# Kernel tuning notes

Hardware: AMD Instinct MI355X
Metric: run time of the kernel (lower is better)

## Reference

```python
import jax, jax.numpy as jnp
import numpy as np


def _gcn(x, src, dst, W, b, n):
    # symmetric normalization: deg computed on edges WITH self-loops (weights 1)
    deg = jax.ops.segment_sum(jnp.ones_like(src, dtype=x.dtype), dst, num_segments=n)
    dinv = jnp.where(deg > 0, jax.lax.rsqrt(deg), 0.0)
    norm = dinv[src] * dinv[dst]              # [E+n]
    xw = x @ W                                # [n, out] transform first (cheaper)
    msg = xw[src] * norm[:, None]             # gather + edge scale
    return jax.ops.segment_sum(msg, dst, num_segments=n) + b


def setup_inputs() -> dict:
    key = jax.random.key(0)
    ks = jax.random.split(key, 8)
    N, E = 100_000, 1_280_000
    x = jax.random.normal(ks[0], (N, 18), dtype=jnp.float32)
    edge_index = jax.random.randint(ks[1], (2, E), 0, N, dtype=jnp.int32)
    W1 = jax.random.normal(ks[2], (18, 32), dtype=jnp.float32) * 0.2
    b1 = jnp.zeros((32,), dtype=jnp.float32)
    W2 = jax.random.normal(ks[3], (32, 64), dtype=jnp.float32) * 0.15
    b2 = jnp.zeros((64,), dtype=jnp.float32)
    Wfc = jax.random.normal(ks[4], (64, 2), dtype=jnp.float32) * 0.1
    bfc = jnp.zeros((2,), dtype=jnp.float32)
    return {"x": x, "edge_index": edge_index, "W1": W1, "b1": b1,
            "W2": W2, "b2": b2, "Wfc": Wfc, "bfc": bfc}


def reference(x, edge_index, W1, b1, W2, b2, Wfc, bfc):
    n = x.shape[0]
    loop = jnp.arange(n, dtype=edge_index.dtype)
    src = jnp.concatenate([edge_index[0], loop])   # add self-loops (PyG default)
    dst = jnp.concatenate([edge_index[1], loop])
    h = jax.nn.relu(_gcn(x, src, dst, W1, b1, n))
    h = jax.nn.relu(_gcn(h, src, dst, W2, b2, n))
    logits = h @ Wfc + bfc
    return jax.nn.log_softmax(logits, axis=1)
```

## Files before the change

kernel.cpp:

```cpp
#include <hip/hip_runtime.h>
#include <hip/hip_fp16.h>
#include <math.h>


#define TPB 256
#define BSH 8
#define BNODES 256
#define MAXBUCK 512
#define CH 8192
#define NPW 8
#define CAPSH 12
#define CAP (1 << CAPSH)

__global__ void k_initcur(int* __restrict__ bcursor, int nbuck) {
    int i = blockIdx.x * blockDim.x + threadIdx.x;
    if (i < nbuck) bcursor[i] = i << CAPSH;
}

__global__ void k_part(const int* __restrict__ src, const int* __restrict__ dst,
                       int* __restrict__ bcursor, int* __restrict__ eb,
                       int E, int nbuck) {
    __shared__ int lh[MAXBUCK];
    __shared__ int lbase[MAXBUCK];
    int t = threadIdx.x;
    int chunk0 = blockIdx.x * CH;
    int end = min(chunk0 + CH, E);
    const int4* dst4 = (const int4*)dst;
    const int4* src4 = (const int4*)src;
    for (int i = t; i < nbuck; i += TPB) lh[i] = 0;
    __syncthreads();
    for (int e4 = chunk0 / 4 + t; e4 * 4 < end; e4 += TPB) {
        int base = e4 * 4;
        int4 d = dst4[e4];
        if (base + 0 < end) atomicAdd(&lh[d.x >> BSH], 1);
        if (base + 1 < end) atomicAdd(&lh[d.y >> BSH], 1);
        if (base + 2 < end) atomicAdd(&lh[d.z >> BSH], 1);
        if (base + 3 < end) atomicAdd(&lh[d.w >> BSH], 1);
    }
    __syncthreads();
    for (int i = t; i < nbuck; i += TPB) {
        int c = lh[i];
        lbase[i] = c ? atomicAdd(&bcursor[i], c) : 0;
        lh[i] = 0;
    }
    __syncthreads();
    for (int e4 = chunk0 / 4 + t; e4 * 4 < end; e4 += TPB) {
        int base = e4 * 4;
        int4 d = dst4[e4];
        int4 s = src4[e4];
        #define PUT(c, sv) if (base + c < end) { \
            int b = (d.sv) >> BSH; \
            int r = atomicAdd(&lh[b], 1); \
            int pos = lbase[b] + r; \
            if (pos < ((b + 1) << CAPSH)) \
                eb[pos] = ((s.sv) << BSH) | ((d.sv) & (BNODES - 1)); }
        PUT(0, x) PUT(1, y) PUT(2, z) PUT(3, w)
        #undef PUT
    }
}

__global__ void k_bucket(const int* __restrict__ eb, const int* __restrict__ bcursor,
                         const float* __restrict__ x,
                         int* __restrict__ csr, int* __restrict__ row_start,
                         int* __restrict__ cnt, float* __restrict__ dinv,
                         __half* __restrict__ u1h, int n) {
    __shared__ int lcnt[BNODES];
    __shared__ int lscan[BNODES];
    __shared__ float ldinv[BNODES];
    int b = blockIdx.x;
    int t = threadIdx.x;
    int node0 = b << BSH;
    int beg = b << CAPSH;
    int end = bcursor[b];
    lcnt[t] = 0;
    __syncthreads();
    for (int i = beg + t; i < end; i += TPB)
        atomicAdd(&lcnt[eb[i] & (BNODES - 1)], 1);
    __syncthreads();
    int v = lcnt[t];
    lscan[t] = v;
    __syncthreads();
    for (int off = 1; off < TPB; off <<= 1) {
        int xx = (t >= off) ? lscan[t - off] : 0;
        __syncthreads();
        lscan[t] += xx;
        __syncthreads();
    }
    int excl = lscan[t] - v;
    int node = node0 + t;
    float dv = rsqrtf(1.0f + (float)v);
    ldinv[t] = dv;
    if (node < n) {
        row_start[node] = beg + excl;
        cnt[node] = v;
        dinv[node] = dv;
    }
    __syncthreads();
    lcnt[t] = excl;
    __syncthreads();
    for (int i = beg + t; i < end; i += TPB) {
        int e = eb[i];
        int p = atomicAdd(&lcnt[e & (BNODES - 1)], 1);
        csr[beg + p] = e >> BSH;
    }
    int nn = min(BNODES, n - node0);
    int tot = nn * 32;
    const float* xb = x + (size_t)node0 * 18;
    __half* ub = u1h + (size_t)node0 * 32;
    for (int i = t; i < tot; i += TPB) {
        int nl = i >> 5, f = i & 31;
        float val = (f < 18) ? xb[nl * 18 + f] * ldinv[nl] : 0.f;
        ub[i] = __float2half_rn(val);
    }
}

template <int OS, int NW>
__global__ void k_agg(const __half2* __restrict__ uh2, const int* __restrict__ row_start,
                      const int* __restrict__ cnt, const int* __restrict__ csr,
                      float* __restrict__ agg, int n) {
    int t = blockIdx.x * blockDim.x + threadIdx.x;
    int node = t >> 4, f2 = t & 15;
    if (node >= n) return;
    int beg = row_start[node], num = cnt[node];
    float2 acc = __half22float2(uh2[(size_t)node * 16 + f2]);
    int i = 0;
    for (; i + 4 <= num; i += 4) {
        int s0 = csr[beg + i], s1 = csr[beg + i + 1];
        int s2 = csr[beg + i + 2], s3 = csr[beg + i + 3];
        float2 v0 = __half22float2(uh2[(size_t)s0 * 16 + f2]);
        float2 v1 = __half22float2(uh2[(size_t)s1 * 16 + f2]);
        float2 v2 = __half22float2(uh2[(size_t)s2 * 16 + f2]);
        float2 v3 = __half22float2(uh2[(size_t)s3 * 16 + f2]);
        acc.x += (v0.x + v1.x) + (v2.x + v3.x);
        acc.y += (v0.y + v1.y) + (v2.y + v3.y);
    }
    for (; i < num; ++i) {
        int s = csr[beg + i];
        float2 v = __half22float2(uh2[(size_t)s * 16 + f2]);
        acc.x += v.x;
        acc.y += v.y;
    }
    if (f2 < NW) *(float2*)(agg + (size_t)node * OS + 2 * f2) = acc;
}

__global__ void k_l1(const float* __restrict__ agg1, const float* __restrict__ W1,
                     const float* __restrict__ dinv, const float* __restrict__ b1,
                     __half* __restrict__ u2h, int n) {
    int lane = threadIdx.x & 63;
    int f = lane & 31;
    int wid = __builtin_amdgcn_readfirstlane((int)(threadIdx.x >> 6));
    int wave = blockIdx.x * (TPB / 64) + wid;
    float w1r[18];
#pragma unroll
    for (int k = 0; k < 18; ++k) w1r[k] = W1[k * 32 + f];
    float b1v = b1[f];
    int node0 = wave * NPW;
    for (int r = 0; r < NPW; ++r) {
        int node = node0 + r;
        if (node >= n) return;
        const float* rp = agg1 + (size_t)node * 18;
        float a = 0.f;
#pragma unroll
        for (int k = 0; k < 18; ++k) a = fmaf(rp[k], w1r[k], a);
        float di = dinv[node];
        if (lane < 32)
            u2h[(size_t)node * 32 + f] =
                __float2half_rn(fmaxf(fmaf(di, a, b1v), 0.f) * di);
    }
}

__global__ void k_l2_out(const float* __restrict__ agg2, const float* __restrict__ W2,
                         const float* __restrict__ dinv, const float* __restrict__ b2,
                         const float* __restrict__ Wfc, const float* __restrict__ bfc,
                         float* __restrict__ out, int n) {
    int lane = threadIdx.x & 63;
    int wid = __builtin_amdgcn_readfirstlane((int)(threadIdx.x >> 6));
    int wave = blockIdx.x * (TPB / 64) + wid;
    float w2r[32];
#pragma unroll
    for (int k = 0; k < 32; ++k) w2r[k] = W2[k * 64 + lane];
    float b2v = b2[lane];
    float wf0 = Wfc[lane * 2 + 0], wf1 = Wfc[lane * 2 + 1];
    float bf0 = bfc[0], bf1 = bfc[1];
    int node0 = wave * NPW;
    for (int r = 0; r < NPW; ++r) {
        int node = node0 + r;
        if (node >= n) return;
        const float* rp = agg2 + (size_t)node * 32;
        float a0 = 0.f, a1 = 0.f, a2 = 0.f, a3 = 0.f;
#pragma unroll
        for (int k = 0; k < 32; k += 4) {
            a0 = fmaf(rp[k],     w2r[k],     a0);
            a1 = fmaf(rp[k + 1], w2r[k + 1], a1);
            a2 = fmaf(rp[k + 2], w2r[k + 2], a2);
            a3 = fmaf(rp[k + 3], w2r[k + 3], a3);
        }
        float a = (a0 + a1) + (a2 + a3);
        float v = fmaxf(fmaf(dinv[node], a, b2v), 0.f);
        float l0 = v * wf0;
        float l1 = v * wf1;
#pragma unroll
        for (int off = 32; off >= 1; off >>= 1) {
            l0 += __shfl_xor(l0, off, 64);
            l1 += __shfl_xor(l1, off, 64);
        }
        if (lane == 0) {
            l0 += bf0;
            l1 += bf1;
            float m2 = fmaxf(l0, l1);
            float lse = m2 + logf(expf(l0 - m2) + expf(l1 - m2));
            out[node * 2 + 0] = l0 - lse;
            out[node * 2 + 1] = l1 - lse;
        }
    }
}

extern "C" void kernel_launch(void* const* d_in, const int* in_sizes, int n_in,
                              void* d_out, int out_size, void* d_ws, size_t ws_size,
                              hipStream_t stream) {
    const float* x   = (const float*)d_in[0];
    const int*   ei  = (const int*)d_in[1];
    const float* W1  = (const float*)d_in[2];
    const float* b1  = (const float*)d_in[3];
    const float* W2  = (const float*)d_in[4];
    const float* b2  = (const float*)d_in[5];
    const float* Wfc = (const float*)d_in[6];
    const float* bfc = (const float*)d_in[7];
    float* out = (float*)d_out;

    const int n = in_sizes[0] / 18;
    const int E = in_sizes[1] / 2;
    const int* src = ei;
    const int* dst = ei + E;
    const int nbuck = (n + BNODES - 1) >> BSH;

    char* w = (char*)d_ws;
    int*    bcursor   = (int*)w;     w += (size_t)nbuck * 4;
    int*    row_start = (int*)w;     w += (size_t)n * 4;
    int*    cnt       = (int*)w;     w += (size_t)n * 4;
    float*  dinv      = (float*)w;   w += (size_t)n * 4;
    int*    eb        = (int*)w;     w += (size_t)nbuck * CAP * 4;
    int*    csr       = (int*)w;     w += (size_t)nbuck * CAP * 4;
    float*  agg1      = (float*)w;   w += (size_t)n * 18 * 4;
    float*  agg2      = (float*)w;   w += (size_t)n * 32 * 4;
    w = (char*)(((size_t)w + 63) & ~(size_t)63);
    __half* u1h       = (__half*)w;  w += (size_t)n * 32 * 2;
    w = (char*)(((size_t)w + 63) & ~(size_t)63);
    __half* u2h       = (__half*)w;  w += (size_t)n * 32 * 2;

    auto blocks = [](long long work) { return (int)((work + TPB - 1) / TPB); };

    k_initcur<<<blocks(nbuck), TPB, 0, stream>>>(bcursor, nbuck);
    k_part<<<(E + CH - 1) / CH, TPB, 0, stream>>>(src, dst, bcursor, eb, E, nbuck);
    k_bucket<<<nbuck, TPB, 0, stream>>>(eb, bcursor, x, csr, row_start, cnt, dinv, u1h, n);

    const int blocksA = blocks((long long)n * 16);
    const int wavesT = (n + NPW - 1) / NPW;
    const int blocksT = (wavesT + (TPB / 64) - 1) / (TPB / 64);

    k_agg<18, 9><<<blocksA, TPB, 0, stream>>>((const __half2*)u1h, row_start, cnt, csr, agg1, n);
    k_l1<<<blocksT, TPB, 0, stream>>>(agg1, W1, dinv, b1, u2h, n);

    k_agg<32, 16><<<blocksA, TPB, 0, stream>>>((const __half2*)u2h, row_start, cnt, csr, agg2, n);
    k_l2_out<<<blocksT, TPB, 0, stream>>>(agg2, W2, dinv, b2, Wfc, bfc, out, n);
}
```

Measured before the change: 196.5 us.

## Fuse neighbor aggregation with dense transforms and replace cursor init with memset

Each layer's gather-aggregation kernel is merged with its dense transform kernel. The aggregated features for 16 nodes are staged in shared memory, and the same block then applies W1 (or W2 plus the FC and log-softmax) in a grid-stride loop. This removes the agg1/agg2 global round trips and two launches. The per-bucket cursor now counts from zero, set by a memset in place of an init kernel, and bucket offsets are computed from the bucket index. The cost is block-level syncs per group, a persistent grid capped at 2048 blocks, and register pressure from the held weights.

```diff
diff --git a/kernel.cpp b/kernel.cpp
--- a/kernel.cpp
+++ b/kernel.cpp
@@ -8,14 +8,8 @@
 #define BNODES 256
 #define MAXBUCK 512
 #define CH 8192
-#define NPW 8
 #define CAPSH 12
 #define CAP (1 << CAPSH)
-
-__global__ void k_initcur(int* __restrict__ bcursor, int nbuck) {
-    int i = blockIdx.x * blockDim.x + threadIdx.x;
-    if (i < nbuck) bcursor[i] = i << CAPSH;
-}
 
 __global__ void k_part(const int* __restrict__ src, const int* __restrict__ dst,
                        int* __restrict__ bcursor, int* __restrict__ eb,
@@ -50,10 +44,9 @@
         int4 s = src4[e4];
         #define PUT(c, sv) if (base + c < end) { \
             int b = (d.sv) >> BSH; \
-            int r = atomicAdd(&lh[b], 1); \
-            int pos = lbase[b] + r; \
-            if (pos < ((b + 1) << CAPSH)) \
-                eb[pos] = ((s.sv) << BSH) | ((d.sv) & (BNODES - 1)); }
+            int r = lbase[b] + atomicAdd(&lh[b], 1); \
+            if (r < CAP) \
+                eb[((size_t)b << CAPSH) + r] = ((s.sv) << BSH) | ((d.sv) & (BNODES - 1)); }
         PUT(0, x) PUT(1, y) PUT(2, z) PUT(3, w)
         #undef PUT
     }
@@ -71,7 +64,7 @@
     int t = threadIdx.x;
     int node0 = b << BSH;
     int beg = b << CAPSH;
-    int end = bcursor[b];
+    int end = beg + min(bcursor[b], CAP);
     lcnt[t] = 0;
     __syncthreads();
     for (int i = beg + t; i < end; i += TPB)
@@ -114,104 +107,141 @@
     }
 }
 
-template <int OS, int NW>
-__global__ void k_agg(const __half2* __restrict__ uh2, const int* __restrict__ row_start,
-                      const int* __restrict__ cnt, const int* __restrict__ csr,
-                      float* __restrict__ agg, int n) {
-    int t = blockIdx.x * blockDim.x + threadIdx.x;
-    int node = t >> 4, f2 = t & 15;
-    if (node >= n) return;
-    int beg = row_start[node], num = cnt[node];
-    float2 acc = __half22float2(uh2[(size_t)node * 16 + f2]);
-    int i = 0;
-    for (; i + 4 <= num; i += 4) {
-        int s0 = csr[beg + i], s1 = csr[beg + i + 1];
-        int s2 = csr[beg + i + 2], s3 = csr[beg + i + 3];
-        float2 v0 = __half22float2(uh2[(size_t)s0 * 16 + f2]);
-        float2 v1 = __half22float2(uh2[(size_t)s1 * 16 + f2]);
-        float2 v2 = __half22float2(uh2[(size_t)s2 * 16 + f2]);
-        float2 v3 = __half22float2(uh2[(size_t)s3 * 16 + f2]);
-        acc.x += (v0.x + v1.x) + (v2.x + v3.x);
-        acc.y += (v0.y + v1.y) + (v2.y + v3.y);
-    }
-    for (; i < num; ++i) {
-        int s = csr[beg + i];
-        float2 v = __half22float2(uh2[(size_t)s * 16 + f2]);
-        acc.x += v.x;
-        acc.y += v.y;
-    }
-    if (f2 < NW) *(float2*)(agg + (size_t)node * OS + 2 * f2) = acc;
-}
-
-__global__ void k_l1(const float* __restrict__ agg1, const float* __restrict__ W1,
-                     const float* __restrict__ dinv, const float* __restrict__ b1,
-                     __half* __restrict__ u2h, int n) {
-    int lane = threadIdx.x & 63;
+__global__ void k_fused1(const __half2* __restrict__ u1h2, const int* __restrict__ row_start,
+                         const int* __restrict__ cnt, const int* __restrict__ csr,
+                         const float* __restrict__ dinv, const float* __restrict__ W1,
+                         const float* __restrict__ b1, __half* __restrict__ u2h,
+                         int n, int ngroups) {
+    __shared__ float lagg[16][19];
+    int t = threadIdx.x;
+    int lane = t & 63, wv = t >> 6;
+    int f2 = t & 15, nl = t >> 4;
     int f = lane & 31;
-    int wid = __builtin_amdgcn_readfirstlane((int)(threadIdx.x >> 6));
-    int wave = blockIdx.x * (TPB / 64) + wid;
     float w1r[18];
 #pragma unroll
     for (int k = 0; k < 18; ++k) w1r[k] = W1[k * 32 + f];
     float b1v = b1[f];
-    int node0 = wave * NPW;
-    for (int r = 0; r < NPW; ++r) {
-        int node = node0 + r;
-        if (node >= n) return;
-        const float* rp = agg1 + (size_t)node * 18;
-        float a = 0.f;
-#pragma unroll
-        for (int k = 0; k < 18; ++k) a = fmaf(rp[k], w1r[k], a);
-        float di = dinv[node];
-        if (lane < 32)
-            u2h[(size_t)node * 32 + f] =
-                __float2half_rn(fmaxf(fmaf(di, a, b1v), 0.f) * di);
-    }
-}
-
-__global__ void k_l2_out(const float* __restrict__ agg2, const float* __restrict__ W2,
-                         const float* __restrict__ dinv, const float* __restrict__ b2,
-                         const float* __restrict__ Wfc, const float* __restrict__ bfc,
-                         float* __restrict__ out, int n) {
-    int lane = threadIdx.x & 63;
-    int wid = __builtin_amdgcn_readfirstlane((int)(threadIdx.x >> 6));
-    int wave = blockIdx.x * (TPB / 64) + wid;
+    for (int g = blockIdx.x; g < ngroups; g += gridDim.x) {
+        int node = g * 16 + nl;
+        float2 acc = make_float2(0.f, 0.f);
+        if (node < n) {
+            acc = __half22float2(u1h2[(size_t)node * 16 + f2]);
+            int beg = row_start[node], num = cnt[node];
+            int i = 0;
+            for (; i + 4 <= num; i += 4) {
+                int s0 = csr[beg + i], s1 = csr[beg + i + 1];
+                int s2 = csr[beg + i + 2], s3 = csr[beg + i + 3];
+                float2 v0 = __half22float2(u1h2[(size_t)s0 * 16 + f2]);
+                float2 v1 = __half22float2(u1h2[(size_t)s1 * 16 + f2]);
+                float2 v2 = __half22float2(u1h2[(size_t)s2 * 16 + f2]);
+                float2 v3 = __half22float2(u1h2[(size_t)s3 * 16 + f2]);
+                acc.x += (v0.x + v1.x) + (v2.x + v3.x);
+                acc.y += (v0.y + v1.y) + (v2.y + v3.y);
+            }
+            for (; i < num; ++i) {
+                int s = csr[beg + i];
+                float2 v = __half22float2(u1h2[(size_t)s * 16 + f2]);
+                acc.x += v.x;
+                acc.y += v.y;
+            }
+        }
+        if (f2 < 9) {
+            lagg[nl][2 * f2] = acc.x;
+            lagg[nl][2 * f2 + 1] = acc.y;
+        }
+        __syncthreads();
+#pragma unroll
+        for (int rr = 0; rr < 4; ++rr) {
+            int nl2 = rr * 4 + wv;
+            int node2 = g * 16 + nl2;
+            if (node2 < n) {
+                float a = 0.f;
+#pragma unroll
+                for (int k = 0; k < 18; ++k) a = fmaf(lagg[nl2][k], w1r[k], a);
+                float di = dinv[node2];
+                if (lane < 32)
+                    u2h[(size_t)node2 * 32 + f] =
+                        __float2half_rn(fmaxf(fmaf(di, a, b1v), 0.f) * di);
+            }
+        }
+        __syncthreads();
+    }
+}
+
+__global__ void k_fused2(const __half2* __restrict__ u2h2, const int* __restrict__ row_start,
+                         const int* __restrict__ cnt, const int* __restrict__ csr,
+                         const float* __restrict__ dinv, const float* __restrict__ W2,
+                         const float* __restrict__ b2, const float* __restrict__ Wfc,
+                         const float* __restrict__ bfc, float* __restrict__ out,
+                         int n, int ngroups) {
+    __shared__ float lagg[16][33];
+    int t = threadIdx.x;
+    int lane = t & 63, wv = t >> 6;
+    int f2 = t & 15, nl = t >> 4;
     float w2r[32];
 #pragma unroll
     for (int k = 0; k < 32; ++k) w2r[k] = W2[k * 64 + lane];
     float b2v = b2[lane];
     float wf0 = Wfc[lane * 2 + 0], wf1 = Wfc[lane * 2 + 1];
     float bf0 = bfc[0], bf1 = bfc[1];
-    int node0 = wave * NPW;
-    for (int r = 0; r < NPW; ++r) {
-        int node = node0 + r;
-        if (node >= n) return;
-        const float* rp = agg2 + (size_t)node * 32;
-        float a0 = 0.f, a1 = 0.f, a2 = 0.f, a3 = 0.f;
-#pragma unroll
-        for (int k = 0; k < 32; k += 4) {
-            a0 = fmaf(rp[k],     w2r[k],     a0);
-            a1 = fmaf(rp[k + 1], w2r[k + 1], a1);
-            a2 = fmaf(rp[k + 2], w2r[k + 2], a2);
-            a3 = fmaf(rp[k + 3], w2r[k + 3], a3);
-        }
-        float a = (a0 + a1) + (a2 + a3);
-        float v = fmaxf(fmaf(dinv[node], a, b2v), 0.f);
-        float l0 = v * wf0;
-        float l1 = v * wf1;
-#pragma unroll
-        for (int off = 32; off >= 1; off >>= 1) {
-            l0 += __shfl_xor(l0, off, 64);
-            l1 += __shfl_xor(l1, off, 64);
-        }
-        if (lane == 0) {
-            l0 += bf0;
-            l1 += bf1;
-            float m2 = fmaxf(l0, l1);
-            float lse = m2 + logf(expf(l0 - m2) + expf(l1 - m2));
-            out[node * 2 + 0] = l0 - lse;
-            out[node * 2 + 1] = l1 - lse;
-        }
+    for (int g = blockIdx.x; g < ngroups; g += gridDim.x) {
+        int node = g * 16 + nl;
+        float2 acc = make_float2(0.f, 0.f);
+        if (node < n) {
+            acc = __half22float2(u2h2[(size_t)node * 16 + f2]);
+            int beg = row_start[node], num = cnt[node];
+            int i = 0;
+            for (; i + 4 <= num; i += 4) {
+                int s0 = csr[beg + i], s1 = csr[beg + i + 1];
+                int s2 = csr[beg + i + 2], s3 = csr[beg + i + 3];
+                float2 v0 = __half22float2(u2h2[(size_t)s0 * 16 + f2]);
+                float2 v1 = __half22float2(u2h2[(size_t)s1 * 16 + f2]);
+                float2 v2 = __half22float2(u2h2[(size_t)s2 * 16 + f2]);
+                float2 v3 = __half22float2(u2h2[(size_t)s3 * 16 + f2]);
+                acc.x += (v0.x + v1.x) + (v2.x + v3.x);
+                acc.y += (v0.y + v1.y) + (v2.y + v3.y);
+            }
+            for (; i < num; ++i) {
+                int s = csr[beg + i];
+                float2 v = __half22float2(u2h2[(size_t)s * 16 + f2]);
+                acc.x += v.x;
+                acc.y += v.y;
+            }
+        }
+        lagg[nl][2 * f2] = acc.x;
+        lagg[nl][2 * f2 + 1] = acc.y;
+        __syncthreads();
+#pragma unroll
+        for (int rr = 0; rr < 4; ++rr) {
+            int nl2 = rr * 4 + wv;
+            int node2 = g * 16 + nl2;
+            float a0 = 0.f, a1 = 0.f, a2 = 0.f, a3 = 0.f;
+#pragma unroll
+            for (int k = 0; k < 32; k += 4) {
+                a0 = fmaf(lagg[nl2][k],     w2r[k],     a0);
+                a1 = fmaf(lagg[nl2][k + 1], w2r[k + 1], a1);
+                a2 = fmaf(lagg[nl2][k + 2], w2r[k + 2], a2);
+                a3 = fmaf(lagg[nl2][k + 3], w2r[k + 3], a3);
+            }
+            float a = (a0 + a1) + (a2 + a3);
+            float v = (node2 < n) ? fmaxf(fmaf(dinv[node2], a, b2v), 0.f) : 0.f;
+            float l0 = v * wf0;
+            float l1 = v * wf1;
+#pragma unroll
+            for (int off = 32; off >= 1; off >>= 1) {
+                l0 += __shfl_xor(l0, off, 64);
+                l1 += __shfl_xor(l1, off, 64);
+            }
+            if (lane == 0 && node2 < n) {
+                l0 += bf0;
+                l1 += bf1;
+                float m2 = fmaxf(l0, l1);
+                float lse = m2 + logf(expf(l0 - m2) + expf(l1 - m2));
+                out[node2 * 2 + 0] = l0 - lse;
+                out[node2 * 2 + 1] = l1 - lse;
+            }
+        }
+        __syncthreads();
     }
 }
 
@@ -241,26 +271,20 @@
     float*  dinv      = (float*)w;   w += (size_t)n * 4;
     int*    eb        = (int*)w;     w += (size_t)nbuck * CAP * 4;
     int*    csr       = (int*)w;     w += (size_t)nbuck * CAP * 4;
-    float*  agg1      = (float*)w;   w += (size_t)n * 18 * 4;
-    float*  agg2      = (float*)w;   w += (size_t)n * 32 * 4;
     w = (char*)(((size_t)w + 63) & ~(size_t)63);
     __half* u1h       = (__half*)w;  w += (size_t)n * 32 * 2;
     w = (char*)(((size_t)w + 63) & ~(size_t)63);
     __half* u2h       = (__half*)w;  w += (size_t)n * 32 * 2;
 
-    auto blocks = [](long long work) { return (int)((work + TPB - 1) / TPB); };
-
-    k_initcur<<<blocks(nbuck), TPB, 0, stream>>>(bcursor, nbuck);
+    hipMemsetAsync(bcursor, 0, (size_t)nbuck * 4, stream);
     k_part<<<(E + CH - 1) / CH, TPB, 0, stream>>>(src, dst, bcursor, eb, E, nbuck);
     k_bucket<<<nbuck, TPB, 0, stream>>>(eb, bcursor, x, csr, row_start, cnt, dinv, u1h, n);
 
-    const int blocksA = blocks((long long)n * 16);
-    const int wavesT = (n + NPW - 1) / NPW;
-    const int blocksT = (wavesT + (TPB / 64) - 1) / (TPB / 64);
-
-    k_agg<18, 9><<<blocksA, TPB, 0, stream>>>((const __half2*)u1h, row_start, cnt, csr, agg1, n);
-    k_l1<<<blocksT, TPB, 0, stream>>>(agg1, W1, dinv, b1, u2h, n);
-
-    k_agg<32, 16><<<blocksA, TPB, 0, stream>>>((const __half2*)u2h, row_start, cnt, csr, agg2, n);
-    k_l2_out<<<blocksT, TPB, 0, stream>>>(agg2, W2, dinv, b2, Wfc, bfc, out, n);
-}
+    const int ngroups = (n + 15) / 16;
+    const int gridL = min(2048, ngroups);
+
+    k_fused1<<<gridL, TPB, 0, stream>>>((const __half2*)u1h, row_start, cnt, csr,
+                                        dinv, W1, b1, u2h, n, ngroups);
+    k_fused2<<<gridL, TPB, 0, stream>>>((const __half2*)u2h, row_start, cnt, csr,
+                                        dinv, W2, b2, Wfc, bfc, out, n, ngroups);
+}
```

Measured after the change: 202.4 us. 1.03x slower.

## Pad CSR rows to multiples of four with dummy zero node for int4 gathers

Applied to the files above, without the earlier changes.

Each node's neighbour list in the CSR is padded to a multiple of four entries. The padding points at an extra zero row appended to u1h and u2h, so the aggregation loop can load indices as int4 with no scalar tail loop. Bucket capacity is doubled and bucket cursors become relative offsets, which lets a memset replace the init kernel. The trade-off is extra workspace, a few wasted gathers of the dummy row per node, and a serial padding-write loop in the bucket kernel.

```diff
diff --git a/kernel.cpp b/kernel.cpp
--- a/kernel.cpp
+++ b/kernel.cpp
@@ -9,20 +9,20 @@
 #define MAXBUCK 512
 #define CH 8192
 #define NPW 8
-#define CAPSH 12
+#define CAPSH 13
 #define CAP (1 << CAPSH)
-
-__global__ void k_initcur(int* __restrict__ bcursor, int nbuck) {
-    int i = blockIdx.x * blockDim.x + threadIdx.x;
-    if (i < nbuck) bcursor[i] = i << CAPSH;
-}
 
 __global__ void k_part(const int* __restrict__ src, const int* __restrict__ dst,
                        int* __restrict__ bcursor, int* __restrict__ eb,
-                       int E, int nbuck) {
+                       __half* __restrict__ u1h, __half* __restrict__ u2h,
+                       int E, int n, int nbuck) {
     __shared__ int lh[MAXBUCK];
     __shared__ int lbase[MAXBUCK];
     int t = threadIdx.x;
+    if (blockIdx.x == 0 && t < 32) {
+        u1h[(size_t)n * 32 + t] = __float2half_rn(0.f);
+        u2h[(size_t)n * 32 + t] = __float2half_rn(0.f);
+    }
     int chunk0 = blockIdx.x * CH;
     int end = min(chunk0 + CH, E);
     const int4* dst4 = (const int4*)dst;
@@ -50,10 +50,9 @@
         int4 s = src4[e4];
         #define PUT(c, sv) if (base + c < end) { \
             int b = (d.sv) >> BSH; \
-            int r = atomicAdd(&lh[b], 1); \
-            int pos = lbase[b] + r; \
-            if (pos < ((b + 1) << CAPSH)) \
-                eb[pos] = ((s.sv) << BSH) | ((d.sv) & (BNODES - 1)); }
+            int r = lbase[b] + atomicAdd(&lh[b], 1); \
+            if (r < CAP) \
+                eb[((size_t)b << CAPSH) + r] = ((s.sv) << BSH) | ((d.sv) & (BNODES - 1)); }
         PUT(0, x) PUT(1, y) PUT(2, z) PUT(3, w)
         #undef PUT
     }
@@ -62,7 +61,7 @@
 __global__ void k_bucket(const int* __restrict__ eb, const int* __restrict__ bcursor,
                          const float* __restrict__ x,
                          int* __restrict__ csr, int* __restrict__ row_start,
-                         int* __restrict__ cnt, float* __restrict__ dinv,
+                         int* __restrict__ cnt4, float* __restrict__ dinv,
                          __half* __restrict__ u1h, int n) {
     __shared__ int lcnt[BNODES];
     __shared__ int lscan[BNODES];
@@ -71,14 +70,15 @@
     int t = threadIdx.x;
     int node0 = b << BSH;
     int beg = b << CAPSH;
-    int end = bcursor[b];
+    int end = beg + min(bcursor[b], CAP);
     lcnt[t] = 0;
     __syncthreads();
     for (int i = beg + t; i < end; i += TPB)
         atomicAdd(&lcnt[eb[i] & (BNODES - 1)], 1);
     __syncthreads();
     int v = lcnt[t];
-    lscan[t] = v;
+    int pad = (v + 3) & ~3;
+    lscan[t] = pad;
     __syncthreads();
     for (int off = 1; off < TPB; off <<= 1) {
         int xx = (t >= off) ? lscan[t - off] : 0;
@@ -86,23 +86,25 @@
         lscan[t] += xx;
         __syncthreads();
     }
-    int excl = lscan[t] - v;
+    int pexcl = lscan[t] - pad;
     int node = node0 + t;
     float dv = rsqrtf(1.0f + (float)v);
     ldinv[t] = dv;
     if (node < n) {
-        row_start[node] = beg + excl;
-        cnt[node] = v;
+        row_start[node] = beg + pexcl;
+        cnt4[node] = pad >> 2;
         dinv[node] = dv;
     }
     __syncthreads();
-    lcnt[t] = excl;
+    lcnt[t] = pexcl;
     __syncthreads();
     for (int i = beg + t; i < end; i += TPB) {
         int e = eb[i];
         int p = atomicAdd(&lcnt[e & (BNODES - 1)], 1);
         csr[beg + p] = e >> BSH;
     }
+    __syncthreads();
+    for (int p = v; p < pad; ++p) csr[beg + pexcl + p] = n;
     int nn = min(BNODES, n - node0);
     int tot = nn * 32;
     const float* xb = x + (size_t)node0 * 18;
@@ -116,29 +118,23 @@
 
 template <int OS, int NW>
 __global__ void k_agg(const __half2* __restrict__ uh2, const int* __restrict__ row_start,
-                      const int* __restrict__ cnt, const int* __restrict__ csr,
+                      const int* __restrict__ cnt4, const int* __restrict__ csr,
                       float* __restrict__ agg, int n) {
     int t = blockIdx.x * blockDim.x + threadIdx.x;
     int node = t >> 4, f2 = t & 15;
     if (node >= n) return;
-    int beg = row_start[node], num = cnt[node];
+    int beg = row_start[node];
+    int it = cnt4[node];
     float2 acc = __half22float2(uh2[(size_t)node * 16 + f2]);
-    int i = 0;
-    for (; i + 4 <= num; i += 4) {
-        int s0 = csr[beg + i], s1 = csr[beg + i + 1];
-        int s2 = csr[beg + i + 2], s3 = csr[beg + i + 3];
-        float2 v0 = __half22float2(uh2[(size_t)s0 * 16 + f2]);
-        float2 v1 = __half22float2(uh2[(size_t)s1 * 16 + f2]);
-        float2 v2 = __half22float2(uh2[(size_t)s2 * 16 + f2]);
-        float2 v3 = __half22float2(uh2[(size_t)s3 * 16 + f2]);
+    const int4* ip = (const int4*)(csr + beg);
+    for (int i = 0; i < it; ++i) {
+        int4 s = ip[i];
+        float2 v0 = __half22float2(uh2[(size_t)s.x * 16 + f2]);
+        float2 v1 = __half22float2(uh2[(size_t)s.y * 16 + f2]);
+        float2 v2 = __half22float2(uh2[(size_t)s.z * 16 + f2]);
+        float2 v3 = __half22float2(uh2[(size_t)s.w * 16 + f2]);
         acc.x += (v0.x + v1.x) + (v2.x + v3.x);
         acc.y += (v0.y + v1.y) + (v2.y + v3.y);
-    }
-    for (; i < num; ++i) {
-        int s = csr[beg + i];
-        float2 v = __half22float2(uh2[(size_t)s * 16 + f2]);
-        acc.x += v.x;
-        acc.y += v.y;
     }
     if (f2 < NW) *(float2*)(agg + (size_t)node * OS + 2 * f2) = acc;
 }
@@ -237,30 +233,30 @@
     char* w = (char*)d_ws;
     int*    bcursor   = (int*)w;     w += (size_t)nbuck * 4;
     int*    row_start = (int*)w;     w += (size_t)n * 4;
-    int*    cnt       = (int*)w;     w += (size_t)n * 4;
+    int*    cnt4      = (int*)w;     w += (size_t)n * 4;
     float*  dinv      = (float*)w;   w += (size_t)n * 4;
     int*    eb        = (int*)w;     w += (size_t)nbuck * CAP * 4;
     int*    csr       = (int*)w;     w += (size_t)nbuck * CAP * 4;
     float*  agg1      = (float*)w;   w += (size_t)n * 18 * 4;
     float*  agg2      = (float*)w;   w += (size_t)n * 32 * 4;
     w = (char*)(((size_t)w + 63) & ~(size_t)63);
-    __half* u1h       = (__half*)w;  w += (size_t)n * 32 * 2;
+    __half* u1h       = (__half*)w;  w += (size_t)(n + 1) * 32 * 2;
     w = (char*)(((size_t)w + 63) & ~(size_t)63);
-    __half* u2h       = (__half*)w;  w += (size_t)n * 32 * 2;
+    __half* u2h       = (__half*)w;  w += (size_t)(n + 1) * 32 * 2;
 
     auto blocks = [](long long work) { return (int)((work + TPB - 1) / TPB); };
 
-    k_initcur<<<blocks(nbuck), TPB, 0, stream>>>(bcursor, nbuck);
-    k_part<<<(E + CH - 1) / CH, TPB, 0, stream>>>(src, dst, bcursor, eb, E, nbuck);
-    k_bucket<<<nbuck, TPB, 0, stream>>>(eb, bcursor, x, csr, row_start, cnt, dinv, u1h, n);
+    hipMemsetAsync(bcursor, 0, (size_t)nbuck * 4, stream);
+    k_part<<<(E + CH - 1) / CH, TPB, 0, stream>>>(src, dst, bcursor, eb, u1h, u2h, E, n, nbuck);
+    k_bucket<<<nbuck, TPB, 0, stream>>>(eb, bcursor, x, csr, row_start, cnt4, dinv, u1h, n);
 
     const int blocksA = blocks((long long)n * 16);
     const int wavesT = (n + NPW - 1) / NPW;
     const int blocksT = (wavesT + (TPB / 64) - 1) / (TPB / 64);
 
-    k_agg<18, 9><<<blocksA, TPB, 0, stream>>>((const __half2*)u1h, row_start, cnt, csr, agg1, n);
+    k_agg<18, 9><<<blocksA, TPB, 0, stream>>>((const __half2*)u1h, row_start, cnt4, csr, agg1, n);
     k_l1<<<blocksT, TPB, 0, stream>>>(agg1, W1, dinv, b1, u2h, n);
 
-    k_agg<32, 16><<<blocksA, TPB, 0, stream>>>((const __half2*)u2h, row_start, cnt, csr, agg2, n);
+    k_agg<32, 16><<<blocksA, TPB, 0, stream>>>((const __half2*)u2h, row_start, cnt4, csr, agg2, n);
     k_l2_out<<<blocksT, TPB, 0, stream>>>(agg2, W2, dinv, b2, Wfc, bfc, out, n);
 }
```

Result: no change. 195.6 us (-0.4%).
